# Kernel tuning notes

Measured on AMD Instinct MI355X. Metric: run time of the kernel, lower is better.

Reference implementation:

```python
import jax, jax.numpy as jnp
import numpy as np

B, D, R = 256, 4096, 8
MAX_R = 2 * R - 1  # static upper bound on radius (torch uses data-dependent max)


def setup_inputs() -> dict:
    key = jax.random.key(0)
    ks = jax.random.split(key, 6)
    x = jax.random.randint(ks[0], (B, D), 0, 2).astype(jnp.float32)  # binary spins
    W = jax.random.normal(ks[1], (D, D), jnp.float32) / np.float32(np.sqrt(D))
    b = jax.random.normal(ks[2], (D,), jnp.float32)
    radius_raw = jax.random.randint(ks[3], (B, 1), 0, MAX_R)  # +1 in reference -> [1, 2R-1]
    gumbel_u = jax.random.uniform(ks[4], (B, D), jnp.float32)
    u = jax.random.uniform(ks[5], (B,), jnp.float32)
    return {"x": x, "W": W, "b": b, "radius_raw": radius_raw, "gumbel_u": gumbel_u, "u": u}


def _model(x, W, b):
    # quadratic pseudo-Boolean energy model: per-sample scalar score
    return 0.5 * jnp.einsum('bi,ij,bj->b', x, W, x) + x @ b


def reference(x, W, b, radius_raw, gumbel_u, u):
    radius = radius_raw + 1                                   # [B,1] in [1, 2R-1]
    r_mask = (jnp.arange(MAX_R)[None, :] < radius).astype(x.dtype)  # [B, MAX_R]

    score_x = _model(x, W, b)                                 # [B]
    grad = jax.lax.stop_gradient(
        jax.grad(lambda xx: _model(xx, W, b).sum())(x))       # [B,D], detached

    delta_x = -(2.0 * x - 1.0)
    score_change_x = delta_x * grad / 2.0                     # logits of proposal

    # multinomial without replacement == Gumbel top-k on the logits
    eps = 1e-10
    g = -jnp.log(-jnp.log(jnp.clip(gumbel_u, eps, 1.0 - eps)))
    _, indices = jax.lax.top_k(score_change_x + g, MAX_R)     # [B, MAX_R]

    rows = jnp.arange(B)[:, None]
    cur_bits = x[rows, indices]                               # gather
    new_bits = 1.0 - cur_bits
    y = x.at[rows, indices].set(r_mask * new_bits + (1.0 - r_mask) * cur_bits)

    delta_y = -(2.0 * y - 1.0)
    score_y = _model(y, W, b)
    score_change_y = delta_y * grad / 2.0

    log_pypx = score_y - score_x
    log_tilde_pxpy = -jnp.sum(grad * (y - x), axis=-1)
    log_zxzy = (jax.scipy.special.logsumexp(score_change_x, axis=-1)
                - jax.scipy.special.logsumexp(score_change_y, axis=-1))
    log_acc = jnp.minimum(log_pypx + log_tilde_pxpy + log_zxzy, 0.0)

    accepted = (jnp.exp(log_acc) > u).astype(x.dtype)[:, None]  # [B,1]
    return y * accepted + (1.0 - accepted) * x
```

## Files before the change

kernel.cpp:

```cpp
#include <hip/hip_runtime.h>

#define Bsz 256
#define Dd  4096
#define MAXR 15
#define FMAX 3.402823466e+38f
#define KSPLIT 2
#define KCHUNK (Dd / KSPLIT)
#define BK 64
#define LSTRIDE 72

typedef short bf16x8 __attribute__((ext_vector_type(8)));
typedef float f32x4  __attribute__((ext_vector_type(4)));

__device__ __forceinline__ unsigned short f2bf(float f) {
    unsigned int u = __float_as_uint(f);
    unsigned int r = (u + 0x7fffu + ((u >> 16) & 1u)) >> 16;
    return (unsigned short)r;
}
__device__ __forceinline__ float bf2f(unsigned short h) {
    return __uint_as_float(((unsigned int)h) << 16);
}

__global__ __launch_bounds__(256) void k_ssym(const float* __restrict__ W,
                                              const float* __restrict__ x,
                                              unsigned short* __restrict__ shi,
                                              unsigned short* __restrict__ slo,
                                              unsigned short* __restrict__ xb) {
    __shared__ float t1[64][68];
    __shared__ float t2[64][68];
    int bid = blockIdx.x;
    int bi = 0;
    while (bid >= 64 - bi) { bid -= 64 - bi; ++bi; }
    const int bj = bi + bid;
    const int i0 = bi * 64, j0 = bj * 64;
    const int tid = threadIdx.x;

    #pragma unroll
    for (int sb = 0; sb < 4; ++sb) {
        int s = sb * 256 + tid;
        int r = s >> 4, q = (s & 15) * 4;
        *(float4*)&t1[r][q] = *(const float4*)(W + (size_t)(i0 + r) * Dd + j0 + q);
        *(float4*)&t2[r][q] = *(const float4*)(W + (size_t)(j0 + r) * Dd + i0 + q);
    }
    __syncthreads();

    const int r = tid >> 2, c0 = (tid & 3) * 16;
    {
        unsigned short vh[16], vl[16];
        #pragma unroll
        for (int k = 0; k < 16; ++k) {
            float s = 0.5f * (t1[r][c0 + k] + t2[c0 + k][r]);
            vh[k] = f2bf(s);
            vl[k] = f2bf(s - bf2f(vh[k]));
        }
        size_t o = (size_t)(i0 + r) * Dd + j0 + c0;
        *(uint4*)(shi + o) = *(const uint4*)&vh[0];
        *(uint4*)(shi + o + 8) = *(const uint4*)&vh[8];
        *(uint4*)(slo + o) = *(const uint4*)&vl[0];
        *(uint4*)(slo + o + 8) = *(const uint4*)&vl[8];
    }
    if (bi != bj) {
        unsigned short vh[16], vl[16];
        #pragma unroll
        for (int k = 0; k < 16; ++k) {
            float s = 0.5f * (t2[r][c0 + k] + t1[c0 + k][r]);
            vh[k] = f2bf(s);
            vl[k] = f2bf(s - bf2f(vh[k]));
        }
        size_t o = (size_t)(j0 + r) * Dd + i0 + c0;
        *(uint4*)(shi + o) = *(const uint4*)&vh[0];
        *(uint4*)(shi + o + 8) = *(const uint4*)&vh[8];
        *(uint4*)(slo + o) = *(const uint4*)&vl[0];
        *(uint4*)(slo + o + 8) = *(const uint4*)&vl[8];
    }

    if (blockIdx.x < 256) {
        const float* xp = x + (size_t)blockIdx.x * 4096;
        unsigned short* xo = xb + (size_t)blockIdx.x * 4096;
        #pragma unroll
        for (int c = 0; c < 4; ++c) {
            int e = c * 1024 + tid * 4;
            float4 v = *(const float4*)(xp + e);
            unsigned short o4[4] = { f2bf(v.x), f2bf(v.y), f2bf(v.z), f2bf(v.w) };
            *(uint2*)(xo + e) = *(const uint2*)o4;
        }
    }
}

__global__ __launch_bounds__(128) void k_gemm(const unsigned short* __restrict__ xb,
                                              const unsigned short* __restrict__ shi,
                                              const unsigned short* __restrict__ slo,
                                              float* __restrict__ part) {
    __shared__ __align__(16) unsigned short As[64 * LSTRIDE];
    __shared__ __align__(16) unsigned short Bh[64 * LSTRIDE];
    __shared__ __align__(16) unsigned short Bl[64 * LSTRIDE];
    const int tid = threadIdx.x;
    const int n0 = blockIdx.x * 64, m0 = blockIdx.y * 64;
    const int kbase = blockIdx.z * KCHUNK;
    const int w = tid >> 6, lane = tid & 63;
    const int ln = lane & 15, quad = lane >> 4;

    size_t ga[4], gb[4];
    int lofs[4];
    #pragma unroll
    for (int j = 0; j < 4; ++j) {
        int s = tid + j * 128;
        int r = s >> 3, g = s & 7;
        ga[j]   = (size_t)(m0 + r) * Dd + kbase + g * 8;
        gb[j]   = (size_t)(n0 + r) * Dd + kbase + g * 8;
        lofs[j] = r * LSTRIDE + g * 8;
    }

    f32x4 acc[4][2];
    #pragma unroll
    for (int mt = 0; mt < 4; ++mt)
        #pragma unroll
        for (int ct = 0; ct < 2; ++ct)
            #pragma unroll
            for (int rr = 0; rr < 4; ++rr) acc[mt][ct][rr] = 0.0f;

    for (int k0 = 0; k0 < KCHUNK; k0 += BK) {
        __syncthreads();
        bf16x8 va[4], vh[4], vl[4];
        #pragma unroll
        for (int j = 0; j < 4; ++j) {
            va[j] = *(const bf16x8*)(xb  + ga[j] + k0);
            vh[j] = *(const bf16x8*)(shi + gb[j] + k0);
            vl[j] = *(const bf16x8*)(slo + gb[j] + k0);
        }
        #pragma unroll
        for (int j = 0; j < 4; ++j) {
            *(bf16x8*)&As[lofs[j]] = va[j];
            *(bf16x8*)&Bh[lofs[j]] = vh[j];
            *(bf16x8*)&Bl[lofs[j]] = vl[j];
        }
        __syncthreads();
        #pragma unroll
        for (int kk = 0; kk < BK; kk += 32) {
            const int gr = (kk >> 3) + quad;
            bf16x8 a[4];
            #pragma unroll
            for (int mt = 0; mt < 4; ++mt)
                a[mt] = *(const bf16x8*)&As[(mt * 16 + ln) * LSTRIDE + gr * 8];
            #pragma unroll
            for (int ct = 0; ct < 2; ++ct) {
                int rb = w * 32 + ct * 16 + ln;
                bf16x8 bh = *(const bf16x8*)&Bh[rb * LSTRIDE + gr * 8];
                bf16x8 bl = *(const bf16x8*)&Bl[rb * LSTRIDE + gr * 8];
                #pragma unroll
                for (int mt = 0; mt < 4; ++mt) {
                    acc[mt][ct] = __builtin_amdgcn_mfma_f32_16x16x32_bf16(a[mt], bh, acc[mt][ct], 0, 0, 0);
                    acc[mt][ct] = __builtin_amdgcn_mfma_f32_16x16x32_bf16(a[mt], bl, acc[mt][ct], 0, 0, 0);
                }
            }
        }
    }
    float* prow = part + (size_t)blockIdx.z * (Bsz * Dd);
    #pragma unroll
    for (int mt = 0; mt < 4; ++mt)
        #pragma unroll
        for (int ct = 0; ct < 2; ++ct)
            #pragma unroll
            for (int rr = 0; rr < 4; ++rr) {
                int m = m0 + mt * 16 + quad * 4 + rr;
                int n = n0 + w * 32 + ct * 16 + ln;
                prow[(size_t)m * Dd + n] = acc[mt][ct][rr];
            }
}

__device__ __forceinline__ float block_max256(float v, float* redf) {
    #pragma unroll
    for (int off = 32; off; off >>= 1) v = fmaxf(v, __shfl_down(v, off));
    __syncthreads();
    if ((threadIdx.x & 63) == 0) redf[threadIdx.x >> 6] = v;
    __syncthreads();
    return fmaxf(fmaxf(redf[0], redf[1]), fmaxf(redf[2], redf[3]));
}
__device__ __forceinline__ float block_sum256(float v, float* redf) {
    #pragma unroll
    for (int off = 32; off; off >>= 1) v += __shfl_down(v, off);
    __syncthreads();
    if ((threadIdx.x & 63) == 0) redf[threadIdx.x >> 6] = v;
    __syncthreads();
    return (redf[0] + redf[1]) + (redf[2] + redf[3]);
}

__global__ __launch_bounds__(256) void k_epilogue(const float* __restrict__ x,
                                                  const float* __restrict__ W,
                                                  const int* __restrict__ radius_raw,
                                                  const float* __restrict__ gu,
                                                  const float* __restrict__ uvec,
                                                  const float* __restrict__ part,
                                                  const float* __restrict__ bias,
                                                  float* __restrict__ out) {
    __shared__ float scx_s[Dd];
    __shared__ float redf[2][4];
    __shared__ int   redi[2][4];
    __shared__ float redsum[4];
    __shared__ int   flips[MAXR];

    const int b = blockIdx.x;
    const int tid = threadIdx.x;
    const float* xrow  = x  + (size_t)b * Dd;
    const float* gurow = gu + (size_t)b * Dd;
    const float* p0 = part + (size_t)b * Dd;
    const float* p1 = part + (size_t)(Bsz + b) * Dd;

    float4 a0[4], a1[4], bs4[4], xv4[4], uu4[4];
    #pragma unroll
    for (int c = 0; c < 4; ++c) {
        int j = c * 1024 + tid * 4;
        a0[c]  = *(const float4*)(p0 + j);
        a1[c]  = *(const float4*)(p1 + j);
        bs4[c] = *(const float4*)(bias + j);
        xv4[c] = *(const float4*)(xrow + j);
        uu4[c] = *(const float4*)(gurow + j);
    }
    float sc[16], ky[16];
    float lmax = -FMAX;
    float lkey = -FMAX; int lidx = 0x7fffffff;
    #pragma unroll
    for (int c = 0; c < 4; ++c) {
        const float* ga = (const float*)&a0[c];
        const float* gb = (const float*)&a1[c];
        const float* gc = (const float*)&bs4[c];
        const float* gx = (const float*)&xv4[c];
        const float* gup = (const float*)&uu4[c];
        #pragma unroll
        for (int e = 0; e < 4; ++e) {
            int r = c * 4 + e;
            float g = ga[e] + gb[e] + gc[e];
            float s = (1.0f - 2.0f * gx[e]) * g * 0.5f;
            float k = s - logf(-logf(fmaxf(gup[e], 1e-10f)));
            sc[r] = s;
            ky[r] = k;
            lmax = fmaxf(lmax, s);
            if (k > lkey) { lkey = k; lidx = c * 1024 + tid * 4 + e; }
        }
        *(float4*)&scx_s[c * 1024 + tid * 4] = *(const float4*)&sc[c * 4];
    }

    float mx = block_max256(lmax, redsum);
    float ls = 0.0f;
    #pragma unroll
    for (int r = 0; r < 16; ++r) ls += expf(sc[r] - mx);
    float sum_x = block_sum256(ls, redsum);
    float lse_x = mx + logf(sum_x);

    const int radius = radius_raw[b] + 1;
    unsigned removed = 0;
    for (int t = 0; t < radius; ++t) {
        float v = lkey; int idx = lidx;
        #pragma unroll
        for (int off = 32; off; off >>= 1) {
            float v2 = __shfl_down(v, off);
            int   i2 = __shfl_down(idx, off);
            if (v2 > v || (v2 == v && i2 < idx)) { v = v2; idx = i2; }
        }
        const int buf = t & 1;
        if ((tid & 63) == 0) { redf[buf][tid >> 6] = v; redi[buf][tid >> 6] = idx; }
        __syncthreads();
        float bv = redf[buf][0]; int bi = redi[buf][0];
        #pragma unroll
        for (int w2 = 1; w2 < 4; ++w2) {
            float v2 = redf[buf][w2]; int i2 = redi[buf][w2];
            if (v2 > bv || (v2 == bv && i2 < bi)) { bv = v2; bi = i2; }
        }
        if (tid == ((bi >> 2) & 255)) {
            removed |= 1u << (((bi >> 10) << 2) | (bi & 3));
            lkey = -FMAX; lidx = 0x7fffffff;
            #pragma unroll
            for (int c = 0; c < 4; ++c)
                #pragma unroll
                for (int e = 0; e < 4; ++e) {
                    int r = c * 4 + e;
                    if (!(removed & (1u << r)) && ky[r] > lkey) {
                        lkey = ky[r]; lidx = c * 1024 + tid * 4 + e;
                    }
                }
        }
        if (tid == 0) flips[t] = bi;
    }
    __syncthreads();

    float delta = 0.0f;
    if (tid < radius) {
        float sv = scx_s[flips[tid]];
        delta = expf(-sv - mx) - expf(sv - mx);
    }
    float sum_y = sum_x + block_sum256(delta, redsum);
    float lse_y = mx + logf(sum_y);

    float ts = 0.0f;
    for (int t = tid; t < radius * radius; t += 256) {
        int p = flips[t / radius], q = flips[t % radius];
        float dp = 1.0f - 2.0f * xrow[p];
        float dq = 1.0f - 2.0f * xrow[q];
        ts += 0.25f * dp * dq * (W[(size_t)p * Dd + q] + W[(size_t)q * Dd + p]);
    }
    float T = block_sum256(ts, redsum);

    float log_acc = fminf(T + lse_x - lse_y, 0.0f);
    int accepted = (expf(log_acc) > uvec[b]) ? 1 : 0;

    float* orow = out + (size_t)b * Dd;
    #pragma unroll
    for (int c = 0; c < 4; ++c)
        *(float4*)(orow + c * 1024 + tid * 4) = xv4[c];
    __syncthreads();
    if (accepted && tid < radius) {
        int p = flips[tid];
        orow[p] = 1.0f - xrow[p];
    }
}

extern "C" void kernel_launch(void* const* d_in, const int* in_sizes, int n_in,
                              void* d_out, int out_size, void* d_ws, size_t ws_size,
                              hipStream_t stream) {
    const float* x          = (const float*)d_in[0];
    const float* W          = (const float*)d_in[1];
    const float* bias       = (const float*)d_in[2];
    const int*   radius_raw = (const int*)d_in[3];
    const float* gu         = (const float*)d_in[4];
    const float* u          = (const float*)d_in[5];
    float* out = (float*)d_out;

    unsigned short* shi = (unsigned short*)d_ws;
    unsigned short* slo = shi + (size_t)Dd * Dd;
    unsigned short* xb  = slo + (size_t)Dd * Dd;
    float*          prt = (float*)(xb + (size_t)Bsz * Dd);

    k_ssym<<<2080, 256, 0, stream>>>(W, x, shi, slo, xb);
    k_gemm<<<dim3(64, 4, KSPLIT), 128, 0, stream>>>(xb, shi, slo, prt);
    k_epilogue<<<Bsz, 256, 0, stream>>>(x, W, radius_raw, gu, u, prt, bias, out);
}
```

Before: 180.9 us.

## Register-prefetch GEMM tiles and raise split-K to four when workspace allows

The GEMM now loads the next K-tile from global memory into registers while the current tile is in LDS and being consumed, so global-load latency overlaps with MFMA work. Split-K grows from 2 to 4 when the workspace is large enough, giving 1024 blocks instead of 512 for better occupancy across CUs. The epilogue sums a variable number of partial buffers, which adds partial-sum traffic. Index math also moves to 32-bit offsets to save address registers.

```diff
diff --git a/kernel.cpp b/kernel.cpp
--- a/kernel.cpp
+++ b/kernel.cpp
@@ -4,8 +4,6 @@
 #define Dd  4096
 #define MAXR 15
 #define FMAX 3.402823466e+38f
-#define KSPLIT 2
-#define KCHUNK (Dd / KSPLIT)
 #define BK 64
 #define LSTRIDE 72
 
@@ -90,24 +88,25 @@
 __global__ __launch_bounds__(128) void k_gemm(const unsigned short* __restrict__ xb,
                                               const unsigned short* __restrict__ shi,
                                               const unsigned short* __restrict__ slo,
-                                              float* __restrict__ part) {
+                                              float* __restrict__ part,
+                                              int kchunk) {
     __shared__ __align__(16) unsigned short As[64 * LSTRIDE];
     __shared__ __align__(16) unsigned short Bh[64 * LSTRIDE];
     __shared__ __align__(16) unsigned short Bl[64 * LSTRIDE];
     const int tid = threadIdx.x;
     const int n0 = blockIdx.x * 64, m0 = blockIdx.y * 64;
-    const int kbase = blockIdx.z * KCHUNK;
+    const int kbase = blockIdx.z * kchunk;
     const int w = tid >> 6, lane = tid & 63;
     const int ln = lane & 15, quad = lane >> 4;
 
-    size_t ga[4], gb[4];
+    unsigned ga[4], gb[4];
     int lofs[4];
     #pragma unroll
     for (int j = 0; j < 4; ++j) {
         int s = tid + j * 128;
         int r = s >> 3, g = s & 7;
-        ga[j]   = (size_t)(m0 + r) * Dd + kbase + g * 8;
-        gb[j]   = (size_t)(n0 + r) * Dd + kbase + g * 8;
+        ga[j]   = (unsigned)((m0 + r) * Dd + kbase + g * 8);
+        gb[j]   = (unsigned)((n0 + r) * Dd + kbase + g * 8);
         lofs[j] = r * LSTRIDE + g * 8;
     }
 
@@ -119,20 +118,31 @@
             #pragma unroll
             for (int rr = 0; rr < 4; ++rr) acc[mt][ct][rr] = 0.0f;
 
-    for (int k0 = 0; k0 < KCHUNK; k0 += BK) {
+    bf16x8 va[4], vh[4], vl[4];
+    #pragma unroll
+    for (int j = 0; j < 4; ++j) {
+        va[j] = *(const bf16x8*)(xb  + ga[j]);
+        vh[j] = *(const bf16x8*)(shi + gb[j]);
+        vl[j] = *(const bf16x8*)(slo + gb[j]);
+    }
+
+    for (int k0 = 0; k0 < kchunk; k0 += BK) {
         __syncthreads();
-        bf16x8 va[4], vh[4], vl[4];
-        #pragma unroll
-        for (int j = 0; j < 4; ++j) {
-            va[j] = *(const bf16x8*)(xb  + ga[j] + k0);
-            vh[j] = *(const bf16x8*)(shi + gb[j] + k0);
-            vl[j] = *(const bf16x8*)(slo + gb[j] + k0);
-        }
         #pragma unroll
         for (int j = 0; j < 4; ++j) {
             *(bf16x8*)&As[lofs[j]] = va[j];
             *(bf16x8*)&Bh[lofs[j]] = vh[j];
             *(bf16x8*)&Bl[lofs[j]] = vl[j];
+        }
+        {
+            int kn = k0 + BK;
+            int ks = (kn < kchunk) ? kn : 0;
+            #pragma unroll
+            for (int j = 0; j < 4; ++j) {
+                va[j] = *(const bf16x8*)(xb  + ga[j] + ks);
+                vh[j] = *(const bf16x8*)(shi + gb[j] + ks);
+                vl[j] = *(const bf16x8*)(slo + gb[j] + ks);
+            }
         }
         __syncthreads();
         #pragma unroll
@@ -192,7 +202,8 @@
                                                   const float* __restrict__ uvec,
                                                   const float* __restrict__ part,
                                                   const float* __restrict__ bias,
-                                                  float* __restrict__ out) {
+                                                  float* __restrict__ out,
+                                                  int nsplit) {
     __shared__ float scx_s[Dd];
     __shared__ float redf[2][4];
     __shared__ int   redi[2][4];
@@ -203,33 +214,37 @@
     const int tid = threadIdx.x;
     const float* xrow  = x  + (size_t)b * Dd;
     const float* gurow = gu + (size_t)b * Dd;
-    const float* p0 = part + (size_t)b * Dd;
-    const float* p1 = part + (size_t)(Bsz + b) * Dd;
-
-    float4 a0[4], a1[4], bs4[4], xv4[4], uu4[4];
+
+    float4 g4[4], bs4[4], xv4[4], uu4[4];
     #pragma unroll
     for (int c = 0; c < 4; ++c) {
         int j = c * 1024 + tid * 4;
-        a0[c]  = *(const float4*)(p0 + j);
-        a1[c]  = *(const float4*)(p1 + j);
+        g4[c]  = *(const float4*)(part + (size_t)b * Dd + j);
         bs4[c] = *(const float4*)(bias + j);
         xv4[c] = *(const float4*)(xrow + j);
         uu4[c] = *(const float4*)(gurow + j);
     }
+    for (int z = 1; z < nsplit; ++z) {
+        const float* pz = part + (size_t)z * (Bsz * Dd) + (size_t)b * Dd;
+        #pragma unroll
+        for (int c = 0; c < 4; ++c) {
+            float4 a = *(const float4*)(pz + c * 1024 + tid * 4);
+            g4[c].x += a.x; g4[c].y += a.y; g4[c].z += a.z; g4[c].w += a.w;
+        }
+    }
     float sc[16], ky[16];
     float lmax = -FMAX;
     float lkey = -FMAX; int lidx = 0x7fffffff;
     #pragma unroll
     for (int c = 0; c < 4; ++c) {
-        const float* ga = (const float*)&a0[c];
-        const float* gb = (const float*)&a1[c];
+        const float* gg = (const float*)&g4[c];
         const float* gc = (const float*)&bs4[c];
         const float* gx = (const float*)&xv4[c];
         const float* gup = (const float*)&uu4[c];
         #pragma unroll
         for (int e = 0; e < 4; ++e) {
             int r = c * 4 + e;
-            float g = ga[e] + gb[e] + gc[e];
+            float g = gg[e] + gc[e];
             float s = (1.0f - 2.0f * gx[e]) * g * 0.5f;
             float k = s - logf(-logf(fmaxf(gup[e], 1e-10f)));
             sc[r] = s;
@@ -330,7 +345,11 @@
     unsigned short* xb  = slo + (size_t)Dd * Dd;
     float*          prt = (float*)(xb + (size_t)Bsz * Dd);
 
+    const size_t fixed = (size_t)2 * Dd * Dd * 2 + (size_t)Bsz * Dd * 2;
+    const int nsplit = (ws_size >= fixed + (size_t)4 * Bsz * Dd * 4) ? 4 : 2;
+    const int kchunk = Dd / nsplit;
+
     k_ssym<<<2080, 256, 0, stream>>>(W, x, shi, slo, xb);
-    k_gemm<<<dim3(64, 4, KSPLIT), 128, 0, stream>>>(xb, shi, slo, prt);
-    k_epilogue<<<Bsz, 256, 0, stream>>>(x, W, radius_raw, gu, u, prt, bias, out);
-}
+    k_gemm<<<dim3(64, 4, nsplit), 128, 0, stream>>>(xb, shi, slo, prt, kchunk);
+    k_epilogue<<<Bsz, 256, 0, stream>>>(x, W, radius_raw, gu, u, prt, bias, out, nsplit);
+}
```

New measurement: 173.4 us (median of 2 runs). 1.04x faster.
